# Optimization experiments

Hardware: AMD Instinct MI355X
Metric: run time of the kernel (lower is better)

## Reference

```python
import jax, jax.numpy as jnp
import numpy as np


def setup_inputs() -> dict:
    key = jax.random.key(0)
    ks = jax.random.split(key, 8)
    B, Tq, S, H = 32, 4, 2048, 1024
    return {
        "query": jax.random.normal(ks[0], (B, Tq, H), dtype=jnp.float32),
        "keys": jax.random.normal(ks[1], (S, B, 2 * H), dtype=jnp.float32),
        "Wa_w": jax.random.normal(ks[2], (H, H), dtype=jnp.float32) * 0.02,
        "Wa_b": jax.random.normal(ks[3], (H,), dtype=jnp.float32) * 0.02,
        "Ua_w": jax.random.normal(ks[4], (H, 2 * H), dtype=jnp.float32) * 0.02,
        "Ua_b": jax.random.normal(ks[5], (H,), dtype=jnp.float32) * 0.02,
        "Va_w": jax.random.normal(ks[6], (1, H), dtype=jnp.float32) * 0.02,
        "Va_b": jax.random.normal(ks[7], (1,), dtype=jnp.float32) * 0.02,
    }


def reference(query, keys, Wa_w, Wa_b, Ua_w, Ua_b, Va_w, Va_b):
    # query: [B, Tq, H] -> last step [B, 1, H]
    q = query[:, -1:, :]
    # keys: [S, B, 2H] -> [B, S, 2H]
    k = jnp.transpose(keys, (1, 0, 2))
    # Additive attention scores: Va(tanh(Wa(q) + Ua(k)))
    wq = q @ Wa_w.T + Wa_b                      # [B, 1, H]
    uk = k @ Ua_w.T + Ua_b                      # [B, S, H]
    scores = jnp.tanh(wq + uk) @ Va_w.T + Va_b  # [B, S, 1]
    scores = jnp.transpose(scores, (0, 2, 1))   # [B, 1, S]
    weights = jax.nn.softmax(scores, axis=-1)   # [B, 1, S]
    context = jnp.einsum('bqs,bsd->bqd', weights, k)  # [B, 1, 2H]
    return (context, weights)
```

## Files before the change

### kernel.cpp

```cpp
#include <hip/hip_runtime.h>
#include <hip/hip_bf16.h>

typedef __attribute__((ext_vector_type(4))) float f32x4;
typedef __attribute__((ext_vector_type(8))) short short8;

#define B_   32
#define S_   2048
#define H_   1024
#define D2_  2048
#define BM   256
#define BN   256
#define BK   64
#define NKT  32
#define TILE_SH 16384

__device__ __forceinline__ short f2bf(float f) {
  unsigned u = __float_as_uint(f);
  u = (u + 0x7fffu + ((u >> 16) & 1u)) >> 16;
  return (short)u;
}

__device__ __forceinline__ short8 cvt8(f32x4 a, f32x4 b) {
  short8 o;
  o[0] = f2bf(a.x); o[1] = f2bf(a.y); o[2] = f2bf(a.z); o[3] = f2bf(a.w);
  o[4] = f2bf(b.x); o[5] = f2bf(b.y); o[6] = f2bf(b.z); o[7] = f2bf(b.w);
  return o;
}

__device__ __forceinline__ float fast_tanh(float x) {
  float e = __builtin_amdgcn_exp2f(x * 2.885390081777927f);
  return 1.0f - 2.0f * __builtin_amdgcn_rcpf(e + 1.0f);
}

__device__ __forceinline__ void gload16(const short* g, short* l) {
  __builtin_amdgcn_global_load_lds((const __attribute__((address_space(1))) void*)g,
                                   (__attribute__((address_space(3))) void*)l, 16, 0, 0);
}

__global__ void k_convert_ua(const float* __restrict__ src, short* __restrict__ dst) {
  int idx = blockIdx.x * 256 + threadIdx.x;
  int wu  = idx & 2047;
  int kt  = (idx >> 11) & 31;
  int nt  = idx >> 16;
  int row = wu >> 3;
  int sl  = wu & 7;
  int q   = sl ^ (row & 7);
  const float* s = src + (size_t)(nt * 256 + row) * D2_ + kt * 64 + q * 8;
  f32x4 a = *(const f32x4*)s;
  f32x4 b = *(const f32x4*)(s + 4);
  *(short8*)(dst + (size_t)idx * 8) = cvt8(a, b);
}

__global__ void k_convert_keys(const float* __restrict__ src, short* __restrict__ dst) {
  int idx = blockIdx.x * 256 + threadIdx.x;
  int wu  = idx & 2047;
  int kt  = (idx >> 11) & 31;
  int mt  = idx >> 16;
  int row = wu >> 3;
  int sl  = wu & 7;
  int q   = sl ^ (row & 7);
  const float* s = src + (size_t)(mt * 256 + row) * D2_ + kt * 64 + q * 8;
  f32x4 a = *(const f32x4*)s;
  f32x4 b = *(const f32x4*)(s + 4);
  *(short8*)(dst + (size_t)idx * 8) = cvt8(a, b);
}

__global__ void k_wq(const float* __restrict__ query, const float* __restrict__ Wa_w,
                     const float* __restrict__ Wa_b, const float* __restrict__ Ua_b,
                     float* __restrict__ wqb) {
  int b = blockIdx.x;
  int hc = blockIdx.y;
  int t = threadIdx.x;
  __shared__ float q[H_];
  for (int i = t; i < H_; i += 256) q[i] = query[(size_t)b * (4 * H_) + 3 * H_ + i];
  __syncthreads();
  int h = hc * 128 + (t >> 1);
  int kh = (t & 1) * 512;
  const float* wr = Wa_w + (size_t)h * H_ + kh;
  float acc = 0.f;
  #pragma unroll 8
  for (int k = 0; k < 512; k += 4) {
    f32x4 wv = *(const f32x4*)(wr + k);
    acc += wv.x * q[kh + k] + wv.y * q[kh + k + 1] + wv.z * q[kh + k + 2] + wv.w * q[kh + k + 3];
  }
  acc += __shfl_xor(acc, 1);
  if ((t & 1) == 0) wqb[b * H_ + h] = acc + Wa_b[h] + Ua_b[h];
}

#define AF_READ(mA, mB)                                         \
  af[0] = *(const short8*)&Ac[aread0 + (mA) * 1024];            \
  af[1] = *(const short8*)&Ac[aread1 + (mA) * 1024];            \
  af[2] = *(const short8*)&Ac[aread0 + (mB) * 1024];            \
  af[3] = *(const short8*)&Ac[aread1 + (mB) * 1024];

#define MFMA16(mA, mB)                                                                            \
  __builtin_amdgcn_s_setprio(1);                                                                  \
  _Pragma("unroll")                                                                               \
  for (int n = 0; n < 4; ++n) {                                                                   \
    acc[mA][n] = __builtin_amdgcn_mfma_f32_16x16x32_bf16(af[0], bf[2*n],   acc[mA][n], 0, 0, 0);  \
    acc[mA][n] = __builtin_amdgcn_mfma_f32_16x16x32_bf16(af[1], bf[2*n+1], acc[mA][n], 0, 0, 0);  \
    acc[mB][n] = __builtin_amdgcn_mfma_f32_16x16x32_bf16(af[2], bf[2*n],   acc[mB][n], 0, 0, 0);  \
    acc[mB][n] = __builtin_amdgcn_mfma_f32_16x16x32_bf16(af[3], bf[2*n+1], acc[mB][n], 0, 0, 0);  \
  }                                                                                               \
  __builtin_amdgcn_s_setprio(0);

#define STAGE4(src_, dst_)                         \
  gload16((src_) + 0 * 4096, (dst_) + 0 * 4096 + wu); \
  gload16((src_) + 1 * 4096, (dst_) + 1 * 4096 + wu); \
  gload16((src_) + 2 * 4096, (dst_) + 2 * 4096 + wu); \
  gload16((src_) + 3 * 4096, (dst_) + 3 * 4096 + wu);

__global__ __launch_bounds__(512, 2) void k_gemm_score(
    const short* __restrict__ keys_bf, const short* __restrict__ uab_t,
    const float* __restrict__ wqb, const float* __restrict__ va,
    float* __restrict__ scores_p) {
  __shared__ short As[2][TILE_SH];
  __shared__ short Bs[2][TILE_SH];

  const int bid = blockIdx.x;
  const int g = (bid & 7) * 128 + (bid >> 3);
  const int mt = g >> 2;
  const int nt = g & 3;
  const int r0 = mt * BM;
  const int h0 = nt * BN;

  const int t = threadIdx.x;
  const int lane = t & 63;
  const int w = t >> 6;
  const int wm = w >> 2;
  const int wn = w & 3;

  f32x4 acc[8][4] = {};

  const short* abase = keys_bf + (size_t)mt * (NKT * TILE_SH) + t * 8;
  const short* bbase = uab_t  + (size_t)nt * (NKT * TILE_SH) + t * 8;
  const int wu = w * 512;

  const int lr = lane & 15;
  const int lq = lane >> 4;
  const int sl0 = lq ^ (lr & 7);
  const int aread0 = (wm * 128 + lr) * 64 + sl0 * 8;
  const int aread1 = aread0 ^ 32;
  const int bread0 = (wn * 64 + lr) * 64 + sl0 * 8;
  const int bread1 = bread0 ^ 32;

  {
    STAGE4(abase, &As[0][0])
    STAGE4(bbase, &Bs[0][0])
    asm volatile("s_waitcnt vmcnt(0)" ::: "memory");
    __builtin_amdgcn_s_barrier();
  }

  #pragma unroll 1
  for (int kt = 0; kt < NKT; ++kt) {
    const int cb = kt & 1;
    const bool stage = (kt < NKT - 1);
    const short* Ac = As[cb];
    const short* Bc = Bs[cb];
    const short* anext = abase + (size_t)(kt + 1) * TILE_SH;
    const short* bnext = bbase + (size_t)(kt + 1) * TILE_SH;
    short* Anb = &As[cb ^ 1][0];
    short* Bnb = &Bs[cb ^ 1][0];
    short8 bf[8], af[4];

    #pragma unroll
    for (int n = 0; n < 4; ++n) {
      bf[2 * n]     = *(const short8*)&Bc[bread0 + n * 1024];
      bf[2 * n + 1] = *(const short8*)&Bc[bread1 + n * 1024];
    }
    AF_READ(0, 1)
    if (stage) { STAGE4(anext, Anb) }
    __builtin_amdgcn_s_barrier();
    asm volatile("s_waitcnt lgkmcnt(0)" ::: "memory");
    MFMA16(0, 1)
    __builtin_amdgcn_s_barrier();

    AF_READ(2, 3)
    if (stage) { STAGE4(bnext, Bnb) }
    __builtin_amdgcn_s_barrier();
    asm volatile("s_waitcnt lgkmcnt(0)" ::: "memory");
    MFMA16(2, 3)
    __builtin_amdgcn_s_barrier();

    AF_READ(4, 5)
    __builtin_amdgcn_s_barrier();
    asm volatile("s_waitcnt lgkmcnt(0)" ::: "memory");
    MFMA16(4, 5)
    __builtin_amdgcn_s_barrier();

    AF_READ(6, 7)
    __builtin_amdgcn_s_barrier();
    asm volatile("s_waitcnt lgkmcnt(0)" ::: "memory");
    MFMA16(6, 7)
    asm volatile("s_waitcnt vmcnt(0)" ::: "memory");
    __builtin_amdgcn_s_barrier();
  }

  const int lgrp = lane >> 4;
  const int lc = lane & 15;
  float vah[4];
  #pragma unroll
  for (int n = 0; n < 4; ++n) vah[n] = va[h0 + wn * 64 + n * 16 + lc];
  #pragma unroll
  for (int m = 0; m < 8; ++m) {
    #pragma unroll
    for (int reg = 0; reg < 4; ++reg) {
      int row = wm * 128 + m * 16 + lgrp * 4 + reg;
      int r = r0 + row;
      int bb = r & (B_ - 1);
      const float* wrow = wqb + bb * H_ + h0 + wn * 64 + lc;
      float s = 0.f;
      #pragma unroll
      for (int n = 0; n < 4; ++n)
        s += vah[n] * fast_tanh(acc[m][n][reg] + wrow[n * 16]);
      s += __shfl_xor(s, 1);
      s += __shfl_xor(s, 2);
      s += __shfl_xor(s, 4);
      s += __shfl_xor(s, 8);
      if (lc == 0) scores_p[(size_t)r * 16 + nt * 4 + wn] = s;
    }
  }
}

__global__ __launch_bounds__(512, 2) void k_gemm_rs(
    const float* __restrict__ keys, const short* __restrict__ uab_t,
    const float* __restrict__ wqb, const float* __restrict__ va,
    float* __restrict__ scores_p) {
  __shared__ short As[2][TILE_SH];
  __shared__ short Bs[2][TILE_SH];
  const int bid = blockIdx.x;
  const int g = (bid & 7) * 128 + (bid >> 3);
  const int mt = g >> 2;
  const int nt = g & 3;
  const int r0 = mt * BM;
  const int h0 = nt * BN;
  const int t = threadIdx.x;
  const int lane = t & 63;
  const int w = t >> 6;
  const int wm = w >> 2;
  const int wn = w & 3;
  f32x4 acc[8][4] = {};
  const int arow = t >> 1;
  const int ahalf = t & 1;
  const float* abase = keys + (size_t)(r0 + arow) * D2_ + ahalf * 32;
  int awoff[4];
  #pragma unroll
  for (int j = 0; j < 4; ++j)
    awoff[j] = arow * 64 + ((((ahalf << 2) | j) ^ (arow & 7)) << 3);
  const short* bbase = uab_t + (size_t)nt * NKT * TILE_SH + t * 8;
  const int wu = w * 512;
  const int lr = lane & 15;
  const int lq = lane >> 4;
  const int sl0 = lq ^ (lr & 7);
  const int aread0 = (wm * 128 + lr) * 64 + sl0 * 8;
  const int aread1 = aread0 ^ 32;
  const int bread0 = (wn * 64 + lr) * 64 + sl0 * 8;
  const int bread1 = bread0 ^ 32;
  {
    f32x4 v[8];
    #pragma unroll
    for (int j = 0; j < 8; ++j) v[j] = *(const f32x4*)(abase + j * 4);
    #pragma unroll
    for (int j = 0; j < 4; ++j)
      *(short8*)&As[0][awoff[j]] = cvt8(v[2 * j], v[2 * j + 1]);
    STAGE4(bbase, &Bs[0][0])
    asm volatile("s_waitcnt vmcnt(0) lgkmcnt(0)" ::: "memory");
    __builtin_amdgcn_s_barrier();
  }
  f32x4 av[8];
  #pragma unroll 1
  for (int kt = 0; kt < NKT; ++kt) {
    const int cb = kt & 1;
    const bool stage = (kt < NKT - 1);
    const float* anext = abase + (kt + 1) * BK;
    const short* bnext = bbase + (size_t)(kt + 1) * TILE_SH;
    short* Bnb = &Bs[cb ^ 1][0];
    const short* Ac = As[cb];
    const short* Bc = Bs[cb];
    short8 bf[8], af[4];
    #pragma unroll
    for (int n = 0; n < 4; ++n) {
      bf[2 * n]     = *(const short8*)&Bc[bread0 + n * 1024];
      bf[2 * n + 1] = *(const short8*)&Bc[bread1 + n * 1024];
    }
    AF_READ(0, 1)
    if (stage) {
      #pragma unroll
      for (int j = 0; j < 8; ++j) av[j] = *(const f32x4*)(anext + j * 4);
    }
    __builtin_amdgcn_s_barrier();
    asm volatile("s_waitcnt lgkmcnt(0)" ::: "memory");
    MFMA16(0, 1)
    __builtin_amdgcn_s_barrier();
    AF_READ(2, 3)
    if (stage) {
      gload16(bnext + 0 * 4096, Bnb + 0 * 4096 + wu);
      gload16(bnext + 1 * 4096, Bnb + 1 * 4096 + wu);
    }
    __builtin_amdgcn_s_barrier();
    asm volatile("s_waitcnt lgkmcnt(0)" ::: "memory");
    MFMA16(2, 3)
    __builtin_amdgcn_s_barrier();
    AF_READ(4, 5)
    if (stage) {
      gload16(bnext + 2 * 4096, Bnb + 2 * 4096 + wu);
      gload16(bnext + 3 * 4096, Bnb + 3 * 4096 + wu);
    }
    __builtin_amdgcn_s_barrier();
    asm volatile("s_waitcnt lgkmcnt(0)" ::: "memory");
    MFMA16(4, 5)
    __builtin_amdgcn_s_barrier();
    AF_READ(6, 7)
    if (stage) {
      #pragma unroll
      for (int j = 0; j < 4; ++j)
        *(short8*)&As[cb ^ 1][awoff[j]] = cvt8(av[2 * j], av[2 * j + 1]);
    }
    __builtin_amdgcn_s_barrier();
    asm volatile("s_waitcnt lgkmcnt(0)" ::: "memory");
    MFMA16(6, 7)
    asm volatile("s_waitcnt vmcnt(0) lgkmcnt(0)" ::: "memory");
    __builtin_amdgcn_s_barrier();
  }
  const int lgrp = lane >> 4;
  const int lc = lane & 15;
  float vah[4];
  #pragma unroll
  for (int n = 0; n < 4; ++n) vah[n] = va[h0 + wn * 64 + n * 16 + lc];
  #pragma unroll
  for (int m = 0; m < 8; ++m) {
    #pragma unroll
    for (int reg = 0; reg < 4; ++reg) {
      int row = wm * 128 + m * 16 + lgrp * 4 + reg;
      int r = r0 + row;
      int bb = r & (B_ - 1);
      const float* wrow = wqb + bb * H_ + h0 + wn * 64 + lc;
      float s = 0.f;
      #pragma unroll
      for (int n = 0; n < 4; ++n)
        s += vah[n] * fast_tanh(acc[m][n][reg] + wrow[n * 16]);
      s += __shfl_xor(s, 1);
      s += __shfl_xor(s, 2);
      s += __shfl_xor(s, 4);
      s += __shfl_xor(s, 8);
      if (lc == 0) scores_p[(size_t)r * 16 + nt * 4 + wn] = s;
    }
  }
}

__global__ void k_softmax(const float* __restrict__ scores_p, float* __restrict__ out) {
  int b = blockIdx.x;
  int t = threadIdx.x;
  __shared__ float sc[S_];
  __shared__ float red[4];
  float lmax = -3.4e38f;
  #pragma unroll
  for (int i = 0; i < 8; ++i) {
    int s = t + i * 256;
    const float* p = scores_p + ((size_t)s * B_ + b) * 16;
    f32x4 p0 = *(const f32x4*)p;
    f32x4 p1 = *(const f32x4*)(p + 4);
    f32x4 p2 = *(const f32x4*)(p + 8);
    f32x4 p3 = *(const f32x4*)(p + 12);
    f32x4 ps = p0 + p1 + p2 + p3;
    float v = ps.x + ps.y + ps.z + ps.w;
    sc[s] = v;
    lmax = fmaxf(lmax, v);
  }
  #pragma unroll
  for (int o = 32; o >= 1; o >>= 1) lmax = fmaxf(lmax, __shfl_xor(lmax, o));
  if ((t & 63) == 0) red[t >> 6] = lmax;
  __syncthreads();
  float gmax = fmaxf(fmaxf(red[0], red[1]), fmaxf(red[2], red[3]));
  __syncthreads();
  float lsum = 0.f;
  #pragma unroll
  for (int i = 0; i < 8; ++i) {
    int s = t + i * 256;
    float e = __builtin_amdgcn_exp2f((sc[s] - gmax) * 1.4426950408889634f);
    sc[s] = e;
    lsum += e;
  }
  #pragma unroll
  for (int o = 32; o >= 1; o >>= 1) lsum += __shfl_xor(lsum, o);
  if ((t & 63) == 0) red[t >> 6] = lsum;
  __syncthreads();
  float inv = 1.0f / (red[0] + red[1] + red[2] + red[3]);
  for (int i = 0; i < 8; ++i) {
    int s = t + i * 256;
    out[(size_t)65536 + b * S_ + s] = sc[s] * inv;
  }
}

__global__ void k_ctx_partial(const float* __restrict__ keys, const float* __restrict__ wts,
                              float* __restrict__ cp) {
  int b = blockIdx.x;
  int dc = blockIdx.y;
  int scn = blockIdx.z;
  int t = threadIdx.x;
  __shared__ float wl[256];
  int s0 = scn * 256;
  wl[t] = wts[b * S_ + s0 + t];
  __syncthreads();
  int d = dc * 1024 + t * 4;
  f32x4 acc = {};
  #pragma unroll 4
  for (int i = 0; i < 256; ++i) {
    int s = s0 + i;
    f32x4 kv = *(const f32x4*)(keys + ((size_t)s * B_ + b) * D2_ + d);
    acc += kv * wl[i];
  }
  *(f32x4*)(cp + ((size_t)scn * B_ + b) * D2_ + d) = acc;
}

__global__ void k_ctx_reduce(const float* __restrict__ cp, float* __restrict__ out) {
  int i = blockIdx.x * 256 + threadIdx.x;
  float s = 0.f;
  #pragma unroll
  for (int j = 0; j < 8; ++j) s += cp[(size_t)j * 65536 + i];
  out[i] = s;
}

extern "C" void kernel_launch(void* const* d_in, const int* in_sizes, int n_in,
                              void* d_out, int out_size, void* d_ws, size_t ws_size,
                              hipStream_t stream) {
  const float* query = (const float*)d_in[0];
  const float* keys  = (const float*)d_in[1];
  const float* Wa_w  = (const float*)d_in[2];
  const float* Wa_b  = (const float*)d_in[3];
  const float* Ua_w  = (const float*)d_in[4];
  const float* Ua_b  = (const float*)d_in[5];
  const float* Va_w  = (const float*)d_in[6];
  float* out = (float*)d_out;
  char* ws = (char*)d_ws;

  const size_t KEYS_BF_BYTES = 268435456ull;
  const size_t TAIL = 11ull * 1024 * 1024;
  bool big = ws_size >= KEYS_BF_BYTES + TAIL;

  if (big) {
    short* keys_bf = (short*)ws;
    char* base = ws + KEYS_BF_BYTES;
    short* uab_t = (short*)(base);
    float* wqb = (float*)(base + 4u * 1024 * 1024);
    float* sp  = (float*)(base + 4u * 1024 * 1024 + 128 * 1024);
    float* cp  = (float*)(base + 8u * 1024 * 1024 + 256 * 1024);

    hipLaunchKernelGGL(k_convert_ua, dim3(1024), dim3(256), 0, stream, Ua_w, uab_t);
    hipLaunchKernelGGL(k_convert_keys, dim3(65536), dim3(256), 0, stream, keys, keys_bf);
    hipLaunchKernelGGL(k_wq, dim3(32, 8), dim3(256), 0, stream, query, Wa_w, Wa_b, Ua_b, wqb);
    hipLaunchKernelGGL(k_gemm_score, dim3(1024), dim3(512), 0, stream, keys_bf, uab_t, wqb, Va_w, sp);
    hipLaunchKernelGGL(k_softmax, dim3(32), dim3(256), 0, stream, sp, out);
    hipLaunchKernelGGL(k_ctx_partial, dim3(32, 2, 8), dim3(256), 0, stream, keys, out + 65536, cp);
    hipLaunchKernelGGL(k_ctx_reduce, dim3(256), dim3(256), 0, stream, cp, out);
  } else {
    short* uab_t = (short*)(ws);
    float* wqb = (float*)(ws + 4u * 1024 * 1024);
    float* sp  = (float*)(ws + 4u * 1024 * 1024 + 128 * 1024);
    float* cp  = (float*)(ws + 8u * 1024 * 1024 + 256 * 1024);

    hipLaunchKernelGGL(k_convert_ua, dim3(1024), dim3(256), 0, stream, Ua_w, uab_t);
    hipLaunchKernelGGL(k_wq, dim3(32, 8), dim3(256), 0, stream, query, Wa_w, Wa_b, Ua_b, wqb);
    hipLaunchKernelGGL(k_gemm_rs, dim3(1024), dim3(512), 0, stream, keys, uab_t, wqb, Va_w, sp);
    hipLaunchKernelGGL(k_softmax, dim3(32), dim3(256), 0, stream, sp, out);
    hipLaunchKernelGGL(k_ctx_partial, dim3(32, 2, 8), dim3(256), 0, stream, keys, out + 65536, cp);
    hipLaunchKernelGGL(k_ctx_reduce, dim3(256), dim3(256), 0, stream, cp, out);
  }
}
```

Measured before the change: 544.4 us.

## Split BK tile into two K-halves and compute context from bf16 keys copy

The bf16 tile layout changes from 64-wide swizzled rows to two 32-wide halves with a new XOR swizzle. The GEMM inner loop now uses four B fragments and reloads them per half, and waits on partial vmcnt. The context kernel now reads the bf16 keys copy instead of the fp32 keys, halving that traffic, and writes 16 partial sums instead of 8. The cost is bf16 rounding of keys in the context output and a larger reduce.

```diff
diff --git a/kernel.cpp b/kernel.cpp
--- a/kernel.cpp
+++ b/kernel.cpp
@@ -14,10 +14,15 @@
 #define NKT  32
 #define TILE_SH 16384
 
+
 __device__ __forceinline__ short f2bf(float f) {
   unsigned u = __float_as_uint(f);
   u = (u + 0x7fffu + ((u >> 16) & 1u)) >> 16;
   return (short)u;
+}
+
+__device__ __forceinline__ float bf2f(short s) {
+  return __uint_as_float(((unsigned)(unsigned short)s) << 16);
 }
 
 __device__ __forceinline__ short8 cvt8(f32x4 a, f32x4 b) {
@@ -42,10 +47,11 @@
   int wu  = idx & 2047;
   int kt  = (idx >> 11) & 31;
   int nt  = idx >> 16;
-  int row = wu >> 3;
-  int sl  = wu & 7;
-  int q   = sl ^ (row & 7);
-  const float* s = src + (size_t)(nt * 256 + row) * D2_ + kt * 64 + q * 8;
+  int kh  = wu >> 10;
+  int row = (wu >> 2) & 255;
+  int sl  = wu & 3;
+  int q   = sl ^ ((row >> 1) & 3);
+  const float* s = src + (size_t)(nt * 256 + row) * D2_ + kt * 64 + kh * 32 + q * 8;
   f32x4 a = *(const f32x4*)s;
   f32x4 b = *(const f32x4*)(s + 4);
   *(short8*)(dst + (size_t)idx * 8) = cvt8(a, b);
@@ -56,10 +62,11 @@
   int wu  = idx & 2047;
   int kt  = (idx >> 11) & 31;
   int mt  = idx >> 16;
-  int row = wu >> 3;
-  int sl  = wu & 7;
-  int q   = sl ^ (row & 7);
-  const float* s = src + (size_t)(mt * 256 + row) * D2_ + kt * 64 + q * 8;
+  int kh  = wu >> 10;
+  int row = (wu >> 2) & 255;
+  int sl  = wu & 3;
+  int q   = sl ^ ((row >> 1) & 3);
+  const float* s = src + (size_t)(mt * 256 + row) * D2_ + kt * 64 + kh * 32 + q * 8;
   f32x4 a = *(const f32x4*)s;
   f32x4 b = *(const f32x4*)(s + 4);
   *(short8*)(dst + (size_t)idx * 8) = cvt8(a, b);
@@ -87,28 +94,16 @@
   if ((t & 1) == 0) wqb[b * H_ + h] = acc + Wa_b[h] + Ua_b[h];
 }
 
-#define AF_READ(mA, mB)                                         \
-  af[0] = *(const short8*)&Ac[aread0 + (mA) * 1024];            \
-  af[1] = *(const short8*)&Ac[aread1 + (mA) * 1024];            \
-  af[2] = *(const short8*)&Ac[aread0 + (mB) * 1024];            \
-  af[3] = *(const short8*)&Ac[aread1 + (mB) * 1024];
-
-#define MFMA16(mA, mB)                                                                            \
-  __builtin_amdgcn_s_setprio(1);                                                                  \
-  _Pragma("unroll")                                                                               \
-  for (int n = 0; n < 4; ++n) {                                                                   \
-    acc[mA][n] = __builtin_amdgcn_mfma_f32_16x16x32_bf16(af[0], bf[2*n],   acc[mA][n], 0, 0, 0);  \
-    acc[mA][n] = __builtin_amdgcn_mfma_f32_16x16x32_bf16(af[1], bf[2*n+1], acc[mA][n], 0, 0, 0);  \
-    acc[mB][n] = __builtin_amdgcn_mfma_f32_16x16x32_bf16(af[2], bf[2*n],   acc[mB][n], 0, 0, 0);  \
-    acc[mB][n] = __builtin_amdgcn_mfma_f32_16x16x32_bf16(af[3], bf[2*n+1], acc[mB][n], 0, 0, 0);  \
-  }                                                                                               \
+#define MFMA_C(mb)                                                                                 \
+  __builtin_amdgcn_s_setprio(1);                                                                   \
+  _Pragma("unroll")                                                                                \
+  for (int n = 0; n < 4; ++n) {                                                                    \
+    _Pragma("unroll")                                                                              \
+    for (int i = 0; i < 4; ++i)                                                                    \
+      acc[(mb) + i][n] =                                                                           \
+          __builtin_amdgcn_mfma_f32_16x16x32_bf16(af[i], bf[n], acc[(mb) + i][n], 0, 0, 0);        \
+  }                                                                                                \
   __builtin_amdgcn_s_setprio(0);
-
-#define STAGE4(src_, dst_)                         \
-  gload16((src_) + 0 * 4096, (dst_) + 0 * 4096 + wu); \
-  gload16((src_) + 1 * 4096, (dst_) + 1 * 4096 + wu); \
-  gload16((src_) + 2 * 4096, (dst_) + 2 * 4096 + wu); \
-  gload16((src_) + 3 * 4096, (dst_) + 3 * 4096 + wu);
 
 __global__ __launch_bounds__(512, 2) void k_gemm_score(
     const short* __restrict__ keys_bf, const short* __restrict__ uab_t,
@@ -138,18 +133,20 @@
 
   const int lr = lane & 15;
   const int lq = lane >> 4;
-  const int sl0 = lq ^ (lr & 7);
-  const int aread0 = (wm * 128 + lr) * 64 + sl0 * 8;
-  const int aread1 = aread0 ^ 32;
-  const int bread0 = (wn * 64 + lr) * 64 + sl0 * 8;
-  const int bread1 = bread0 ^ 32;
+  const int slot = lq ^ ((lr >> 1) & 3);
+  const int ar_ = (wm * 128 + lr) * 32 + slot * 8;
+  const int br_ = (wn * 64 + lr) * 32 + slot * 8;
 
   {
-    STAGE4(abase, &As[0][0])
-    STAGE4(bbase, &Bs[0][0])
+    #pragma unroll
+    for (int j = 0; j < 4; ++j) gload16(abase + j * 4096, &As[0][j * 4096 + wu]);
+    #pragma unroll
+    for (int j = 0; j < 4; ++j) gload16(bbase + j * 4096, &Bs[0][j * 4096 + wu]);
     asm volatile("s_waitcnt vmcnt(0)" ::: "memory");
     __builtin_amdgcn_s_barrier();
   }
+
+  short8 af[4], bf[4];
 
   #pragma unroll 1
   for (int kt = 0; kt < NKT; ++kt) {
@@ -161,38 +158,56 @@
     const short* bnext = bbase + (size_t)(kt + 1) * TILE_SH;
     short* Anb = &As[cb ^ 1][0];
     short* Bnb = &Bs[cb ^ 1][0];
-    short8 bf[8], af[4];
-
-    #pragma unroll
-    for (int n = 0; n < 4; ++n) {
-      bf[2 * n]     = *(const short8*)&Bc[bread0 + n * 1024];
-      bf[2 * n + 1] = *(const short8*)&Bc[bread1 + n * 1024];
-    }
-    AF_READ(0, 1)
-    if (stage) { STAGE4(anext, Anb) }
-    __builtin_amdgcn_s_barrier();
-    asm volatile("s_waitcnt lgkmcnt(0)" ::: "memory");
-    MFMA16(0, 1)
-    __builtin_amdgcn_s_barrier();
-
-    AF_READ(2, 3)
-    if (stage) { STAGE4(bnext, Bnb) }
-    __builtin_amdgcn_s_barrier();
-    asm volatile("s_waitcnt lgkmcnt(0)" ::: "memory");
-    MFMA16(2, 3)
-    __builtin_amdgcn_s_barrier();
-
-    AF_READ(4, 5)
-    __builtin_amdgcn_s_barrier();
-    asm volatile("s_waitcnt lgkmcnt(0)" ::: "memory");
-    MFMA16(4, 5)
-    __builtin_amdgcn_s_barrier();
-
-    AF_READ(6, 7)
-    __builtin_amdgcn_s_barrier();
-    asm volatile("s_waitcnt lgkmcnt(0)" ::: "memory");
-    MFMA16(6, 7)
-    asm volatile("s_waitcnt vmcnt(0)" ::: "memory");
+
+    #pragma unroll
+    for (int n = 0; n < 4; ++n) bf[n] = *(const short8*)&Bc[br_ + n * 512];
+    #pragma unroll
+    for (int i = 0; i < 4; ++i) af[i] = *(const short8*)&Ac[ar_ + i * 512];
+    if (stage) {
+      gload16(anext + 0 * 4096, Anb + 0 * 4096 + wu);
+      gload16(anext + 1 * 4096, Anb + 1 * 4096 + wu);
+    }
+    __builtin_amdgcn_s_barrier();
+    asm volatile("s_waitcnt lgkmcnt(0)" ::: "memory");
+    MFMA_C(0)
+    __builtin_amdgcn_s_barrier();
+
+    #pragma unroll
+    for (int i = 0; i < 4; ++i) af[i] = *(const short8*)&Ac[ar_ + (4 + i) * 512];
+    if (stage) {
+      gload16(bnext + 0 * 4096, Bnb + 0 * 4096 + wu);
+      gload16(bnext + 1 * 4096, Bnb + 1 * 4096 + wu);
+    }
+    __builtin_amdgcn_s_barrier();
+    asm volatile("s_waitcnt lgkmcnt(0)" ::: "memory");
+    MFMA_C(4)
+    if (stage) { asm volatile("s_waitcnt vmcnt(4)" ::: "memory"); }
+    else       { asm volatile("s_waitcnt vmcnt(0)" ::: "memory"); }
+    __builtin_amdgcn_s_barrier();
+
+    #pragma unroll
+    for (int n = 0; n < 4; ++n) bf[n] = *(const short8*)&Bc[br_ + 8192 + n * 512];
+    #pragma unroll
+    for (int i = 0; i < 4; ++i) af[i] = *(const short8*)&Ac[ar_ + 8192 + i * 512];
+    if (stage) {
+      gload16(anext + 2 * 4096, Anb + 2 * 4096 + wu);
+      gload16(anext + 3 * 4096, Anb + 3 * 4096 + wu);
+    }
+    __builtin_amdgcn_s_barrier();
+    asm volatile("s_waitcnt lgkmcnt(0)" ::: "memory");
+    MFMA_C(0)
+    __builtin_amdgcn_s_barrier();
+
+    #pragma unroll
+    for (int i = 0; i < 4; ++i) af[i] = *(const short8*)&Ac[ar_ + 8192 + (4 + i) * 512];
+    if (stage) {
+      gload16(bnext + 2 * 4096, Bnb + 2 * 4096 + wu);
+      gload16(bnext + 3 * 4096, Bnb + 3 * 4096 + wu);
+    }
+    __builtin_amdgcn_s_barrier();
+    asm volatile("s_waitcnt lgkmcnt(0)" ::: "memory");
+    MFMA_C(4)
+    if (stage) { asm volatile("s_waitcnt vmcnt(4)" ::: "memory"); }
     __builtin_amdgcn_s_barrier();
   }
 
@@ -246,16 +261,14 @@
   int awoff[4];
   #pragma unroll
   for (int j = 0; j < 4; ++j)
-    awoff[j] = arow * 64 + ((((ahalf << 2) | j) ^ (arow & 7)) << 3);
+    awoff[j] = (ahalf * 1024 + arow * 4 + (j ^ ((arow >> 1) & 3))) * 8;
   const short* bbase = uab_t + (size_t)nt * NKT * TILE_SH + t * 8;
   const int wu = w * 512;
   const int lr = lane & 15;
   const int lq = lane >> 4;
-  const int sl0 = lq ^ (lr & 7);
-  const int aread0 = (wm * 128 + lr) * 64 + sl0 * 8;
-  const int aread1 = aread0 ^ 32;
-  const int bread0 = (wn * 64 + lr) * 64 + sl0 * 8;
-  const int bread1 = bread0 ^ 32;
+  const int slot = lq ^ ((lr >> 1) & 3);
+  const int ar_ = (wm * 128 + lr) * 32 + slot * 8;
+  const int br_ = (wn * 64 + lr) * 32 + slot * 8;
   {
     f32x4 v[8];
     #pragma unroll
@@ -263,11 +276,13 @@
     #pragma unroll
     for (int j = 0; j < 4; ++j)
       *(short8*)&As[0][awoff[j]] = cvt8(v[2 * j], v[2 * j + 1]);
-    STAGE4(bbase, &Bs[0][0])
+    #pragma unroll
+    for (int j = 0; j < 4; ++j) gload16(bbase + j * 4096, &Bs[0][j * 4096 + wu]);
     asm volatile("s_waitcnt vmcnt(0) lgkmcnt(0)" ::: "memory");
     __builtin_amdgcn_s_barrier();
   }
   f32x4 av[8];
+  short8 af[4], bf[4];
   #pragma unroll 1
   for (int kt = 0; kt < NKT; ++kt) {
     const int cb = kt & 1;
@@ -277,40 +292,46 @@
     short* Bnb = &Bs[cb ^ 1][0];
     const short* Ac = As[cb];
     const short* Bc = Bs[cb];
-    short8 bf[8], af[4];
-    #pragma unroll
-    for (int n = 0; n < 4; ++n) {
-      bf[2 * n]     = *(const short8*)&Bc[bread0 + n * 1024];
-      bf[2 * n + 1] = *(const short8*)&Bc[bread1 + n * 1024];
-    }
-    AF_READ(0, 1)
+
+    #pragma unroll
+    for (int n = 0; n < 4; ++n) bf[n] = *(const short8*)&Bc[br_ + n * 512];
+    #pragma unroll
+    for (int i = 0; i < 4; ++i) af[i] = *(const short8*)&Ac[ar_ + i * 512];
     if (stage) {
       #pragma unroll
       for (int j = 0; j < 8; ++j) av[j] = *(const f32x4*)(anext + j * 4);
     }
     __builtin_amdgcn_s_barrier();
     asm volatile("s_waitcnt lgkmcnt(0)" ::: "memory");
-    MFMA16(0, 1)
-    __builtin_amdgcn_s_barrier();
-    AF_READ(2, 3)
+    MFMA_C(0)
+    __builtin_amdgcn_s_barrier();
+
+    #pragma unroll
+    for (int i = 0; i < 4; ++i) af[i] = *(const short8*)&Ac[ar_ + (4 + i) * 512];
     if (stage) {
       gload16(bnext + 0 * 4096, Bnb + 0 * 4096 + wu);
       gload16(bnext + 1 * 4096, Bnb + 1 * 4096 + wu);
     }
     __builtin_amdgcn_s_barrier();
     asm volatile("s_waitcnt lgkmcnt(0)" ::: "memory");
-    MFMA16(2, 3)
-    __builtin_amdgcn_s_barrier();
-    AF_READ(4, 5)
+    MFMA_C(4)
+    __builtin_amdgcn_s_barrier();
+
+    #pragma unroll
+    for (int n = 0; n < 4; ++n) bf[n] = *(const short8*)&Bc[br_ + 8192 + n * 512];
+    #pragma unroll
+    for (int i = 0; i < 4; ++i) af[i] = *(const short8*)&Ac[ar_ + 8192 + i * 512];
     if (stage) {
       gload16(bnext + 2 * 4096, Bnb + 2 * 4096 + wu);
       gload16(bnext + 3 * 4096, Bnb + 3 * 4096 + wu);
     }
     __builtin_amdgcn_s_barrier();
     asm volatile("s_waitcnt lgkmcnt(0)" ::: "memory");
-    MFMA16(4, 5)
-    __builtin_amdgcn_s_barrier();
-    AF_READ(6, 7)
+    MFMA_C(0)
+    __builtin_amdgcn_s_barrier();
+
+    #pragma unroll
+    for (int i = 0; i < 4; ++i) af[i] = *(const short8*)&Ac[ar_ + 8192 + (4 + i) * 512];
     if (stage) {
       #pragma unroll
       for (int j = 0; j < 4; ++j)
@@ -318,7 +339,7 @@
     }
     __builtin_amdgcn_s_barrier();
     asm volatile("s_waitcnt lgkmcnt(0)" ::: "memory");
-    MFMA16(6, 7)
+    MFMA_C(4)
     asm volatile("s_waitcnt vmcnt(0) lgkmcnt(0)" ::: "memory");
     __builtin_amdgcn_s_barrier();
   }
@@ -390,6 +411,42 @@
     int s = t + i * 256;
     out[(size_t)65536 + b * S_ + s] = sc[s] * inv;
   }
+}
+
+__global__ __launch_bounds__(256) void k_ctx_partial_bf(const short* __restrict__ keys_bf,
+                                                        const float* __restrict__ wts,
+                                                        float* __restrict__ cp) {
+  int b = blockIdx.x;
+  int scn2 = blockIdx.y;
+  int t = threadIdx.x;
+  __shared__ float wl[128];
+  int s0 = scn2 * 128;
+  if (t < 128) wl[t] = wts[b * S_ + s0 + t];
+  __syncthreads();
+  const int k = t * 8;
+  const int kt = k >> 6;
+  const int kh = (k >> 5) & 1;
+  const int q  = (k >> 3) & 3;
+  const int slot = q ^ ((b >> 1) & 3);
+  int roff[8];
+  #pragma unroll
+  for (int j = 0; j < 8; ++j) roff[j] = (j * 32 + b) * 32 + slot * 8;
+  f32x4 accA = {}, accB = {};
+  for (int c = 0; c < 16; ++c) {
+    const short* tb = keys_bf + ((size_t)((scn2 * 16 + c) * 32 + kt) * 2048 + (size_t)kh * 1024) * 8;
+    #pragma unroll
+    for (int j = 0; j < 8; ++j) {
+      short8 v = *(const short8*)(tb + roff[j]);
+      float wgt = wl[c * 8 + j];
+      accA.x += wgt * bf2f(v[0]); accA.y += wgt * bf2f(v[1]);
+      accA.z += wgt * bf2f(v[2]); accA.w += wgt * bf2f(v[3]);
+      accB.x += wgt * bf2f(v[4]); accB.y += wgt * bf2f(v[5]);
+      accB.z += wgt * bf2f(v[6]); accB.w += wgt * bf2f(v[7]);
+    }
+  }
+  float* o = cp + ((size_t)scn2 * B_ + b) * D2_ + k;
+  *(f32x4*)o = accA;
+  *(f32x4*)(o + 4) = accB;
 }
 
 __global__ void k_ctx_partial(const float* __restrict__ keys, const float* __restrict__ wts,
@@ -413,11 +470,10 @@
   *(f32x4*)(cp + ((size_t)scn * B_ + b) * D2_ + d) = acc;
 }
 
-__global__ void k_ctx_reduce(const float* __restrict__ cp, float* __restrict__ out) {
+__global__ void k_ctx_reduce(const float* __restrict__ cp, float* __restrict__ out, int np) {
   int i = blockIdx.x * 256 + threadIdx.x;
   float s = 0.f;
-  #pragma unroll
-  for (int j = 0; j < 8; ++j) s += cp[(size_t)j * 65536 + i];
+  for (int j = 0; j < np; ++j) s += cp[(size_t)j * 65536 + i];
   out[i] = s;
 }
 
@@ -435,7 +491,7 @@
   char* ws = (char*)d_ws;
 
   const size_t KEYS_BF_BYTES = 268435456ull;
-  const size_t TAIL = 11ull * 1024 * 1024;
+  const size_t TAIL = 16ull * 1024 * 1024;
   bool big = ws_size >= KEYS_BF_BYTES + TAIL;
 
   if (big) {
@@ -451,8 +507,8 @@
     hipLaunchKernelGGL(k_wq, dim3(32, 8), dim3(256), 0, stream, query, Wa_w, Wa_b, Ua_b, wqb);
     hipLaunchKernelGGL(k_gemm_score, dim3(1024), dim3(512), 0, stream, keys_bf, uab_t, wqb, Va_w, sp);
     hipLaunchKernelGGL(k_softmax, dim3(32), dim3(256), 0, stream, sp, out);
-    hipLaunchKernelGGL(k_ctx_partial, dim3(32, 2, 8), dim3(256), 0, stream, keys, out + 65536, cp);
-    hipLaunchKernelGGL(k_ctx_reduce, dim3(256), dim3(256), 0, stream, cp, out);
+    hipLaunchKernelGGL(k_ctx_partial_bf, dim3(32, 16), dim3(256), 0, stream, keys_bf, out + 65536, cp);
+    hipLaunchKernelGGL(k_ctx_reduce, dim3(256), dim3(256), 0, stream, cp, out, 16);
   } else {
     short* uab_t = (short*)(ws);
     float* wqb = (float*)(ws + 4u * 1024 * 1024);
@@ -464,6 +520,6 @@
     hipLaunchKernelGGL(k_gemm_rs, dim3(1024), dim3(512), 0, stream, keys, uab_t, wqb, Va_w, sp);
     hipLaunchKernelGGL(k_softmax, dim3(32), dim3(256), 0, stream, sp, out);
     hipLaunchKernelGGL(k_ctx_partial, dim3(32, 2, 8), dim3(256), 0, stream, keys, out + 65536, cp);
-    hipLaunchKernelGGL(k_ctx_reduce, dim3(256), dim3(256), 0, stream, cp, out);
-  }
-}
+    hipLaunchKernelGGL(k_ctx_reduce, dim3(256), dim3(256), 0, stream, cp, out, 8);
+  }
+}
```

Result: no change. 551.0 us (+1.2%).
